# Performance work log

Hardware: AMD Instinct MI355X
Metric: run time of the kernel (lower is better)

Reference implementation:

```python
import jax, jax.numpy as jnp
import numpy as np

B, N, C, H = 16, 576, 768, 12
HD = C // H
SCALE = HD ** -0.5


def setup_inputs() -> dict:
    key = jax.random.key(0)
    ks = jax.random.split(key, 8)
    s = lambda fan: 1.0 / np.sqrt(fan)
    return {
        "x": jax.random.normal(ks[0], (B, N, C), jnp.float32),
        "Wqkv": jax.random.normal(ks[1], (3 * C, C), jnp.float32) * s(C),
        "Wl": jax.random.normal(ks[2], (H, H), jnp.float32) * s(H),
        "bl": jax.random.normal(ks[3], (H,), jnp.float32) * 0.02,
        "Ww": jax.random.normal(ks[4], (H, H), jnp.float32) * s(H),
        "bw": jax.random.normal(ks[5], (H,), jnp.float32) * 0.02,
        "Wproj": jax.random.normal(ks[6], (C, C), jnp.float32) * s(C),
        "bproj": jax.random.normal(ks[7], (C,), jnp.float32) * 0.02,
    }


def reference(x, Wqkv, Wl, bl, Ww, bw, Wproj, bproj):
    b, n, c = x.shape
    # qkv projection: (B,N,3C) -> (3,B,H,N,HD)
    qkv = (x @ Wqkv.T).reshape(b, n, 3, H, HD)
    qkv = jnp.transpose(qkv, (2, 0, 3, 1, 4))
    q, k, v = qkv[0] * SCALE, qkv[1], qkv[2]
    # raw scores (B,H,N,N)
    attn = jnp.einsum("bhmd,bhnd->bhmn", q, k)
    # talking-heads pre-softmax mix over head axis (nn.Linear: y = x @ W.T + b)
    attn = jnp.einsum("bhmn,gh->bgmn", attn, Wl) + bl[None, :, None, None]
    attn = jax.nn.softmax(attn, axis=-1)
    # talking-heads post-softmax mix
    attn = jnp.einsum("bhmn,gh->bgmn", attn, Ww) + bw[None, :, None, None]
    # attn @ V -> (B,N,C)
    out = jnp.einsum("bhmn,bhnd->bhmd", attn, v)
    out = jnp.transpose(out, (0, 2, 1, 3)).reshape(b, n, c)
    return out @ Wproj.T + bproj
```

## Files before the change

kernel.cpp:

```cpp
#include <hip/hip_runtime.h>

#define B_ 16
#define N_ 576
#define C_ 768
#define H_ 12
#define HD_ 64
#define M_ (B_*N_)
#define C3_ (3*C_)
#define KC_ 3
#define NT_ 18

typedef _Float16 f16;
typedef _Float16 f16x8 __attribute__((ext_vector_type(8)));
typedef _Float16 f16x4 __attribute__((ext_vector_type(4)));
typedef float f32x4 __attribute__((ext_vector_type(4)));
typedef float f32x2 __attribute__((ext_vector_type(2)));

__global__ void cvt_f32_f16(const float* __restrict__ in, f16* __restrict__ out, int n4) {
    int i = blockIdx.x * blockDim.x + threadIdx.x;
    int stride = gridDim.x * blockDim.x;
    for (; i < n4; i += stride) {
        float4 v = ((const float4*)in)[i];
        f16x4 o = { (f16)v.x, (f16)v.y, (f16)v.z, (f16)v.w };
        ((f16x4*)out)[i] = o;
    }
}

__device__ __forceinline__ int swz(int row, int slot) {
    return row * 32 + ((slot ^ ((row >> 1) & 3)) * 8);
}

__device__ __forceinline__ void gload16(const void* g, void* l) {
    __builtin_amdgcn_global_load_lds((const __attribute__((address_space(1))) void*)g,
                                     (__attribute__((address_space(3))) void*)l, 16, 0, 0);
}

__device__ __forceinline__ size_t qk_frag_off(int bh12, int t16, int half, int l) {
    return (((size_t)bh12 * 36 + t16) * 2 + half) * 512 + (size_t)l * 8;
}

__global__ __launch_bounds__(256) void gemm_qkv(const f16* __restrict__ A, const f16* __restrict__ Bw,
                                                f16* __restrict__ Qf, f16* __restrict__ Kf, f16* __restrict__ Vo) {
    __shared__ __align__(16) f16 lA[128 * 32];
    __shared__ __align__(16) f16 lB[128 * 32];
    __shared__ __align__(16) f16 eT[4][16][72];
    const int K = C_;
    int m0 = blockIdx.x * 128, n0 = blockIdx.y * 128;
    int t = threadIdx.x, lane = t & 63, wave = t >> 6;
    int wm = (wave >> 1) * 64, wn = (wave & 1) * 64;
    int srow0 = wave * 16 + (lane >> 2);
    int scol0 = ((lane & 3) ^ ((srow0 >> 1) & 3)) * 8;
    int srow1 = srow0 + 64;
    int scol1 = ((lane & 3) ^ ((srow1 >> 1) & 3)) * 8;
    f16* dA0 = lA + wave * 512 + lane * 8;
    f16* dA1 = lA + 2048 + wave * 512 + lane * 8;
    f16* dB0 = lB + wave * 512 + lane * 8;
    f16* dB1 = lB + 2048 + wave * 512 + lane * 8;
    const f16* A0 = A + (size_t)(m0 + srow0) * K + scol0;
    const f16* A1 = A + (size_t)(m0 + srow1) * K + scol1;
    const f16* B0 = Bw + (size_t)(n0 + srow0) * K + scol0;
    const f16* B1 = Bw + (size_t)(n0 + srow1) * K + scol1;
    f32x4 acc[4][4] = {};
    for (int k0 = 0; k0 < K; k0 += 32) {
        gload16(A0 + k0, dA0);
        gload16(A1 + k0, dA1);
        gload16(B0 + k0, dB0);
        gload16(B1 + k0, dB1);
        __syncthreads();
        f16x8 af[4], bf[4];
#pragma unroll
        for (int i = 0; i < 4; ++i) {
            af[i] = *(const f16x8*)(lA + swz(wm + i * 16 + (lane & 15), lane >> 4));
            bf[i] = *(const f16x8*)(lB + swz(wn + i * 16 + (lane & 15), lane >> 4));
        }
#pragma unroll
        for (int i = 0; i < 4; ++i)
#pragma unroll
            for (int j = 0; j < 4; ++j)
                acc[i][j] = __builtin_amdgcn_mfma_f32_16x16x32_f16(af[i], bf[j], acc[i][j], 0, 0, 0);
        __syncthreads();
    }
    int colw = n0 + wn;
    int tsel = colw / C_;
    int rem = colw - tsel * C_;
    int h = rem >> 6;
    float qs = (tsel == 0) ? 0.125f : 1.0f;
#pragma unroll
    for (int i = 0; i < 4; ++i) {
        int rowg = m0 + wm + i * 16;
        int bb = rowg / N_;
        int nnb = rowg - bb * N_;
        int bh = bb * H_ + h;
#pragma unroll
        for (int j = 0; j < 4; ++j)
#pragma unroll
            for (int r = 0; r < 4; ++r)
                eT[wave][(lane >> 4) * 4 + r][j * 16 + (lane & 15)] = (f16)(acc[i][j][r] * qs);
        if (tsel < 2) {
            f16* dst = (tsel == 0) ? Qf : Kf;
#pragma unroll
            for (int half = 0; half < 2; ++half) {
                f16x8 v = *(const f16x8*)&eT[wave][lane & 15][half * 32 + (lane >> 4) * 8];
                *(f16x8*)(dst + qk_frag_off(bh, nnb >> 4, half, lane)) = v;
            }
        } else {
#pragma unroll
            for (int hh = 0; hh < 2; ++hh) {
                int nl = hh * 8 + (lane >> 3);
                f16x8 v = *(const f16x8*)&eT[wave][nl][(lane & 7) * 8];
                *(f16x8*)(Vo + ((size_t)bh * N_ + nnb + nl) * HD_ + (lane & 7) * 8) = v;
            }
        }
    }
}

__global__ __launch_bounds__(256) void gemm_proj(const f16* __restrict__ A, const f16* __restrict__ Bw,
                                                 const float* __restrict__ bias, float* __restrict__ out) {
    __shared__ __align__(16) f16 lA[128 * 32];
    __shared__ __align__(16) f16 lB[128 * 32];
    const int K = C_;
    const size_t PSZ = (size_t)M_ * C_;
    int m0 = blockIdx.x * 128, n0 = blockIdx.y * 128;
    int t = threadIdx.x, lane = t & 63, wave = t >> 6;
    int wm = (wave >> 1) * 64, wn = (wave & 1) * 64;
    int srow = t >> 2, sslot = t & 3, scol = sslot * 8;
    f32x4 acc[4][4] = {};
    for (int k0 = 0; k0 < K; k0 += 32) {
        {
            size_t i0 = (size_t)(m0 + srow) * K + k0 + scol;
            size_t i1 = (size_t)(m0 + srow + 64) * K + k0 + scol;
            f16x8 a0 = *(const f16x8*)(A + i0), a1 = *(const f16x8*)(A + PSZ + i0), a2 = *(const f16x8*)(A + 2 * PSZ + i0);
            *(f16x8*)(lA + swz(srow, sslot)) = a0 + a1 + a2;
            f16x8 b0 = *(const f16x8*)(A + i1), b1 = *(const f16x8*)(A + PSZ + i1), b2 = *(const f16x8*)(A + 2 * PSZ + i1);
            *(f16x8*)(lA + swz(srow + 64, sslot)) = b0 + b1 + b2;
        }
        *(f16x8*)(lB + swz(srow,      sslot)) = *(const f16x8*)(Bw + (size_t)(n0 + srow)      * K + k0 + scol);
        *(f16x8*)(lB + swz(srow + 64, sslot)) = *(const f16x8*)(Bw + (size_t)(n0 + srow + 64) * K + k0 + scol);
        __syncthreads();
        f16x8 af[4], bf[4];
#pragma unroll
        for (int i = 0; i < 4; ++i) {
            af[i] = *(const f16x8*)(lA + swz(wm + i * 16 + (lane & 15), lane >> 4));
            bf[i] = *(const f16x8*)(lB + swz(wn + i * 16 + (lane & 15), lane >> 4));
        }
#pragma unroll
        for (int i = 0; i < 4; ++i)
#pragma unroll
            for (int j = 0; j < 4; ++j)
                acc[i][j] = __builtin_amdgcn_mfma_f32_16x16x32_f16(af[i], bf[j], acc[i][j], 0, 0, 0);
        __syncthreads();
    }
#pragma unroll
    for (int i = 0; i < 4; ++i) {
        int row0 = m0 + wm + i * 16 + ((lane >> 4) * 4);
#pragma unroll
        for (int j = 0; j < 4; ++j) {
            int col = n0 + wn + j * 16 + (lane & 15);
            float bv = bias[col];
#pragma unroll
            for (int r = 0; r < 4; ++r)
                out[(size_t)(row0 + r) * C_ + col] = acc[i][j][r] + bv;
        }
    }
}

__global__ void transpose_v(const f16* __restrict__ V, f16* __restrict__ Vf) {
    __shared__ f16 tile[64][68];
    int bh = blockIdx.y, n0 = blockIdx.x * 64;
    const f16* src = V + (size_t)bh * N_ * HD_;
    int t = threadIdx.x;
#pragma unroll
    for (int i = 0; i < 16; ++i) {
        int e = i * 256 + t;
        int r = e >> 6, c = e & 63;
        tile[r][c] = src[(size_t)(n0 + r) * HD_ + c];
    }
    __syncthreads();
#pragma unroll
    for (int i = 0; i < 2; ++i) {
        int u = i * 256 + t;
        int nt2 = u >> 8, dt = (u >> 6) & 3, l = u & 63;
        int nl = nt2 * 32 + ((l >> 4) << 3);
        int d = dt * 16 + (l & 15);
        f16x8 v;
#pragma unroll
        for (int j = 0; j < 8; ++j) v[j] = tile[nl + j][d];
        size_t off = (((size_t)bh * 18 + (n0 >> 5) + nt2) * 4 + dt) * 512 + (size_t)l * 8;
        *(f16x8*)(Vf + off) = v;
    }
}

__global__ __launch_bounds__(256) void scores_exp(const f16* __restrict__ Qf, const f16* __restrict__ Kf,
                                                  const float* __restrict__ Wl, const float* __restrict__ bl,
                                                  unsigned char* __restrict__ Sp, float* __restrict__ rps) {
    __shared__ float sWl[144];
    __shared__ float sbl[12];
    __shared__ float red[12][32][2];
    int fl = blockIdx.x;
    int xcd = fl & 7;
    int j = fl >> 3;
    int hi = (j >= 324) ? 1 : 0;
    int b = xcd * 2 + hi;
    int j2 = j - hi * 324;
    int p = j2 / 54;
    int rr2 = j2 - p * 54;
    int xt = p * 3 + (rr2 % 3);
    int yt = rr2 / 3;
    int t = threadIdx.x, lane = t & 63, wave = t >> 6;
    int mh = wave >> 1, nh = wave & 1;
    if (t < 144) sWl[t] = Wl[t];
    if (t >= 192 && t < 204) sbl[t - 192] = bl[t - 192];
    __syncthreads();
    int m16 = lane & 15, q = lane >> 4;
    int mt16 = xt * 2 + mh;
    int nt16 = yt * 2 + nh;
    f32x4 S[12];
#pragma unroll
    for (int h = 0; h < 12; ++h) {
        int bh = b * H_ + h;
        f16x8 k0 = *(const f16x8*)(Kf + qk_frag_off(bh, nt16, 0, lane));
        f16x8 k1 = *(const f16x8*)(Kf + qk_frag_off(bh, nt16, 1, lane));
        f16x8 q0 = *(const f16x8*)(Qf + qk_frag_off(bh, mt16, 0, lane));
        f16x8 q1 = *(const f16x8*)(Qf + qk_frag_off(bh, mt16, 1, lane));
        f32x4 a = {0.f, 0.f, 0.f, 0.f};
        a = __builtin_amdgcn_mfma_f32_16x16x32_f16(k0, q0, a, 0, 0, 0);
        a = __builtin_amdgcn_mfma_f32_16x16x32_f16(k1, q1, a, 0, 0, 0);
        S[h] = a;
    }
    int oct = nh * 2 + (q >> 1);
    int lp = m16 | (oct << 4);
    int jo = (q & 1) * 4;
    unsigned char* spb = Sp + ((((size_t)b * 36 + mt16) * 18 + yt) * 12) * 512 + lp * 8 + jo;
    float sg[12];
#pragma unroll
    for (int g = 0; g < 12; ++g) {
        float bg = sbl[g];
        f32x4 w = {bg, bg, bg, bg};
#pragma unroll
        for (int h = 0; h < 12; ++h) w += sWl[g * 12 + h] * S[h];
        float e0 = __expf(w[0]), e1 = __expf(w[1]), e2 = __expf(w[2]), e3 = __expf(w[3]);
        sg[g] = e0 + e1 + e2 + e3;
        unsigned int pk = 0;
        pk = __builtin_amdgcn_cvt_pk_fp8_f32(e0 * 0.25f, e1 * 0.25f, pk, false);
        pk = __builtin_amdgcn_cvt_pk_fp8_f32(e2 * 0.25f, e3 * 0.25f, pk, true);
        *(unsigned int*)(spb + g * 512) = pk;
    }
#pragma unroll
    for (int g = 0; g < 12; ++g) {
        float v = sg[g];
        v += __shfl_xor(v, 16, 64);
        v += __shfl_xor(v, 32, 64);
        if (lane < 16) red[g][mh * 16 + lane][nh] = v;
    }
    __syncthreads();
    for (int tt = t; tt < 384; tt += 256) {
        int g = tt >> 5, mr = tt & 31;
        float tot = red[g][mr][0] + red[g][mr][1];
        rps[(((size_t)b * H_ + g) * N_ + xt * 32 + mr) * NT_ + yt] = tot;
    }
}

__global__ __launch_bounds__(256) void sum_rinv(const float* __restrict__ rps, float* __restrict__ rinv) {
    int row = blockIdx.x * 256 + threadIdx.x;
    const float* p = rps + (size_t)row * NT_;
    float s = 0.f;
#pragma unroll
    for (int i = 0; i < NT_; ++i) s += p[i];
    rinv[row] = 1.0f / s;
}

__global__ __launch_bounds__(256) void pv_mix(const unsigned char* __restrict__ Sp, const f16* __restrict__ Vf,
                                              const float* __restrict__ Ww, const float* __restrict__ bw,
                                              const float* __restrict__ rinv, f16* __restrict__ Opart) {
    __shared__ float ils[12][16];
    int fl = blockIdx.x;
    int sw = (fl & 7) * 216 + (fl >> 3);
    int mt = sw % 36, rem = sw / 36;
    int b = rem & 15, kc = rem >> 4;
    int m0 = mt * 16;
    int t = threadIdx.x, lane = t & 63;
    int wv = __builtin_amdgcn_readfirstlane(t >> 6);
    if (t < 192) ils[t / 16][t % 16] = rinv[((size_t)b * H_ + t / 16) * N_ + m0 + (t % 16)];
    __syncthreads();
    int mrow = lane & 15, n8 = lane >> 4;
    float il_[12];
#pragma unroll
    for (int h = 0; h < 12; ++h) il_[h] = 4.0f * ils[h][mrow];
    float ww0[12], ww1[12], ww2[12];
#pragma unroll
    for (int h = 0; h < 12; ++h) {
        ww0[h] = Ww[(wv * 3 + 0) * H_ + h];
        ww1[h] = Ww[(wv * 3 + 1) * H_ + h];
        ww2[h] = Ww[(wv * 3 + 2) * H_ + h];
    }
    float bw0 = bw[wv * 3], bw1 = bw[wv * 3 + 1], bw2 = bw[wv * 3 + 2];
    const unsigned char* spf = Sp + (((size_t)b * 36 + mt) * 18 + kc * 6) * 6144;
    const f16* vfb = Vf + ((((size_t)b * 12 + wv * 3) * 18 + kc * 6) * 4) * 512;
    f32x4 O[3][4] = {};
    for (int it = 0; it < 6; ++it) {
        uint2 ck8[12];
#pragma unroll
        for (int c = 0; c < 12; ++c)
            ck8[c] = *(const uint2*)(spf + (size_t)(it * 12 + c) * 512 + lane * 8);
        float w0[8], w1[8], w2[8];
#pragma unroll
        for (int jj = 0; jj < 8; ++jj) { w0[jj] = bw0; w1[jj] = bw1; w2[jj] = bw2; }
#pragma unroll
        for (int h = 0; h < 12; ++h) {
            float il = il_[h];
            float c0 = ww0[h], c1 = ww1[h], c2 = ww2[h];
            f32x2 eA = __builtin_amdgcn_cvt_pk_f32_fp8(ck8[h].x, false);
            f32x2 eB = __builtin_amdgcn_cvt_pk_f32_fp8(ck8[h].x, true);
            f32x2 eC = __builtin_amdgcn_cvt_pk_f32_fp8(ck8[h].y, false);
            f32x2 eD = __builtin_amdgcn_cvt_pk_f32_fp8(ck8[h].y, true);
            float p0 = eA.x * il, p1 = eA.y * il, p2 = eB.x * il, p3 = eB.y * il;
            float p4 = eC.x * il, p5 = eC.y * il, p6 = eD.x * il, p7 = eD.y * il;
            w0[0] += c0 * p0; w0[1] += c0 * p1; w0[2] += c0 * p2; w0[3] += c0 * p3;
            w0[4] += c0 * p4; w0[5] += c0 * p5; w0[6] += c0 * p6; w0[7] += c0 * p7;
            w1[0] += c1 * p0; w1[1] += c1 * p1; w1[2] += c1 * p2; w1[3] += c1 * p3;
            w1[4] += c1 * p4; w1[5] += c1 * p5; w1[6] += c1 * p6; w1[7] += c1 * p7;
            w2[0] += c2 * p0; w2[1] += c2 * p1; w2[2] += c2 * p2; w2[3] += c2 * p3;
            w2[4] += c2 * p4; w2[5] += c2 * p5; w2[6] += c2 * p6; w2[7] += c2 * p7;
        }
        f16x8 af0, af1, af2;
#pragma unroll
        for (int jj = 0; jj < 8; ++jj) {
            af0[jj] = (f16)w0[jj]; af1[jj] = (f16)w1[jj]; af2[jj] = (f16)w2[jj];
        }
#pragma unroll
        for (int dt = 0; dt < 4; ++dt) {
            f16x8 bf0 = *(const f16x8*)(vfb + (size_t)0 * 36864 + it * 2048 + dt * 512 + lane * 8);
            O[0][dt] = __builtin_amdgcn_mfma_f32_16x16x32_f16(af0, bf0, O[0][dt], 0, 0, 0);
            f16x8 bf1 = *(const f16x8*)(vfb + (size_t)1 * 36864 + it * 2048 + dt * 512 + lane * 8);
            O[1][dt] = __builtin_amdgcn_mfma_f32_16x16x32_f16(af1, bf1, O[1][dt], 0, 0, 0);
            f16x8 bf2 = *(const f16x8*)(vfb + (size_t)2 * 36864 + it * 2048 + dt * 512 + lane * 8);
            O[2][dt] = __builtin_amdgcn_mfma_f32_16x16x32_f16(af2, bf2, O[2][dt], 0, 0, 0);
        }
    }
    f16* Ob = Opart + (size_t)kc * M_ * C_;
#pragma unroll
    for (int gi = 0; gi < 3; ++gi) {
        int g = wv * 3 + gi;
#pragma unroll
        for (int dt = 0; dt < 4; ++dt)
#pragma unroll
            for (int r = 0; r < 4; ++r)
                Ob[((size_t)b * N_ + m0 + n8 * 4 + r) * C_ + g * HD_ + dt * 16 + mrow] = (f16)O[gi][dt][r];
    }
}

extern "C" void kernel_launch(void* const* d_in, const int* in_sizes, int n_in,
                              void* d_out, int out_size, void* d_ws, size_t ws_size,
                              hipStream_t stream) {
    const float* x     = (const float*)d_in[0];
    const float* Wqkv  = (const float*)d_in[1];
    const float* Wl    = (const float*)d_in[2];
    const float* bl    = (const float*)d_in[3];
    const float* Ww    = (const float*)d_in[4];
    const float* bw    = (const float*)d_in[5];
    const float* Wproj = (const float*)d_in[6];
    const float* bproj = (const float*)d_in[7];
    float* out = (float*)d_out;

    char* ws = (char*)d_ws;
    size_t off = 0;
    auto alloc = [&](size_t bytes) -> void* {
        void* p = ws + off;
        off += (bytes + 255) & ~(size_t)255;
        return p;
    };
    f16* x_h  = (f16*)alloc((size_t)M_ * C_ * 2);
    f16* wq_h = (f16*)alloc((size_t)C3_ * C_ * 2);
    f16* wp_h = (f16*)alloc((size_t)C_ * C_ * 2);
    f16* qf_h = (f16*)alloc((size_t)B_ * H_ * N_ * HD_ * 2);
    f16* kf_h = (f16*)alloc((size_t)B_ * H_ * N_ * HD_ * 2);
    f16* v_h  = (f16*)alloc((size_t)B_ * H_ * N_ * HD_ * 2);
    f16* vf_h = (f16*)alloc((size_t)B_ * H_ * N_ * HD_ * 2);
    unsigned char* sp = (unsigned char*)alloc((size_t)B_ * N_ * N_ * 12);
    float* rps  = (float*)alloc((size_t)B_ * H_ * N_ * NT_ * 4);
    float* rinv = (float*)alloc((size_t)B_ * H_ * N_ * 4);
    f16* opart = (f16*)alloc((size_t)KC_ * M_ * C_ * 2);

    cvt_f32_f16<<<1024, 256, 0, stream>>>(x,     x_h,  M_ * C_ / 4);
    cvt_f32_f16<<<1024, 256, 0, stream>>>(Wqkv,  wq_h, C3_ * C_ / 4);
    cvt_f32_f16<<<512,  256, 0, stream>>>(Wproj, wp_h, C_ * C_ / 4);

    gemm_qkv<<<dim3(M_ / 128, C3_ / 128), 256, 0, stream>>>(x_h, wq_h, qf_h, kf_h, v_h);
    transpose_v<<<dim3(N_ / 64, B_ * H_), 256, 0, stream>>>(v_h, vf_h);
    scores_exp<<<5184, 256, 0, stream>>>(qf_h, kf_h, Wl, bl, sp, rps);
    sum_rinv<<<(B_ * H_ * N_) / 256, 256, 0, stream>>>(rps, rinv);
    pv_mix<<<36 * 16 * KC_, 256, 0, stream>>>(sp, vf_h, Ww, bw, rinv, opart);
    gemm_proj<<<dim3(M_ / 128, C_ / 128), 256, 0, stream>>>(opart, wp_h, bproj, out);
}
```

Baseline: 211.5 us.

## Stage K fragments in LDS for larger score tiles; async-load proj weights

The scores kernel moves to 512-thread blocks covering 64 query rows. Each block stages its 12 heads of K fragments in shared memory once and reuses them across four query tiles, instead of every wave reading K from global memory. The row-sum reduction buffer is switched to half precision to save shared memory, which may lose some accuracy in the softmax denominators. Separately, gemm_proj now loads its weight tiles with direct global-to-LDS loads rather than through registers, so those loads are issued earlier and no register staging is needed.

```diff
diff --git a/kernel.cpp b/kernel.cpp
--- a/kernel.cpp
+++ b/kernel.cpp
@@ -124,8 +124,18 @@
     int t = threadIdx.x, lane = t & 63, wave = t >> 6;
     int wm = (wave >> 1) * 64, wn = (wave & 1) * 64;
     int srow = t >> 2, sslot = t & 3, scol = sslot * 8;
+    int brow0 = wave * 16 + (lane >> 2);
+    int bcol0 = ((lane & 3) ^ ((brow0 >> 1) & 3)) * 8;
+    int brow1 = brow0 + 64;
+    int bcol1 = ((lane & 3) ^ ((brow1 >> 1) & 3)) * 8;
+    f16* dB0 = lB + wave * 512 + lane * 8;
+    f16* dB1 = lB + 2048 + wave * 512 + lane * 8;
+    const f16* B0 = Bw + (size_t)(n0 + brow0) * K + bcol0;
+    const f16* B1 = Bw + (size_t)(n0 + brow1) * K + bcol1;
     f32x4 acc[4][4] = {};
     for (int k0 = 0; k0 < K; k0 += 32) {
+        gload16(B0 + k0, dB0);
+        gload16(B1 + k0, dB1);
         {
             size_t i0 = (size_t)(m0 + srow) * K + k0 + scol;
             size_t i1 = (size_t)(m0 + srow + 64) * K + k0 + scol;
@@ -134,8 +144,6 @@
             f16x8 b0 = *(const f16x8*)(A + i1), b1 = *(const f16x8*)(A + PSZ + i1), b2 = *(const f16x8*)(A + 2 * PSZ + i1);
             *(f16x8*)(lA + swz(srow + 64, sslot)) = b0 + b1 + b2;
         }
-        *(f16x8*)(lB + swz(srow,      sslot)) = *(const f16x8*)(Bw + (size_t)(n0 + srow)      * K + k0 + scol);
-        *(f16x8*)(lB + swz(srow + 64, sslot)) = *(const f16x8*)(Bw + (size_t)(n0 + srow + 64) * K + k0 + scol);
         __syncthreads();
         f16x8 af[4], bf[4];
 #pragma unroll
@@ -190,36 +198,44 @@
     }
 }
 
-__global__ __launch_bounds__(256) void scores_exp(const f16* __restrict__ Qf, const f16* __restrict__ Kf,
+__global__ __launch_bounds__(512) void scores_exp(const f16* __restrict__ Qf, const f16* __restrict__ Kf,
                                                   const float* __restrict__ Wl, const float* __restrict__ bl,
                                                   unsigned char* __restrict__ Sp, float* __restrict__ rps) {
     __shared__ float sWl[144];
     __shared__ float sbl[12];
-    __shared__ float red[12][32][2];
+    __shared__ f16 red[12][64][2];
+    __shared__ __align__(16) f16 lK[2 * 12 * 2 * 512];
     int fl = blockIdx.x;
     int xcd = fl & 7;
     int j = fl >> 3;
-    int hi = (j >= 324) ? 1 : 0;
+    int hi = (j >= 162) ? 1 : 0;
     int b = xcd * 2 + hi;
-    int j2 = j - hi * 324;
-    int p = j2 / 54;
-    int rr2 = j2 - p * 54;
-    int xt = p * 3 + (rr2 % 3);
-    int yt = rr2 / 3;
+    int j2 = j - hi * 162;
+    int yt = j2 / 9;
+    int mb = j2 - yt * 9;
     int t = threadIdx.x, lane = t & 63, wave = t >> 6;
-    int mh = wave >> 1, nh = wave & 1;
+    int mh = wave >> 2 ? 0 : 0;
+    mh = wave >> 1;
+    int nh = wave & 1;
     if (t < 144) sWl[t] = Wl[t];
     if (t >= 192 && t < 204) sbl[t - 192] = bl[t - 192];
+#pragma unroll
+    for (int i = 0; i < 6; ++i) {
+        int c = wave * 6 + i;
+        int nh2 = c / 24, rest = c - nh2 * 24;
+        int h = rest >> 1, half = rest & 1;
+        gload16(Kf + qk_frag_off(b * H_ + h, yt * 2 + nh2, half, 0) + (size_t)lane * 8,
+                lK + c * 512 + lane * 8);
+    }
     __syncthreads();
     int m16 = lane & 15, q = lane >> 4;
-    int mt16 = xt * 2 + mh;
-    int nt16 = yt * 2 + nh;
+    int mt16 = mb * 4 + mh;
     f32x4 S[12];
 #pragma unroll
     for (int h = 0; h < 12; ++h) {
         int bh = b * H_ + h;
-        f16x8 k0 = *(const f16x8*)(Kf + qk_frag_off(bh, nt16, 0, lane));
-        f16x8 k1 = *(const f16x8*)(Kf + qk_frag_off(bh, nt16, 1, lane));
+        f16x8 k0 = *(const f16x8*)(lK + ((nh * 12 + h) * 2 + 0) * 512 + lane * 8);
+        f16x8 k1 = *(const f16x8*)(lK + ((nh * 12 + h) * 2 + 1) * 512 + lane * 8);
         f16x8 q0 = *(const f16x8*)(Qf + qk_frag_off(bh, mt16, 0, lane));
         f16x8 q1 = *(const f16x8*)(Qf + qk_frag_off(bh, mt16, 1, lane));
         f32x4 a = {0.f, 0.f, 0.f, 0.f};
@@ -250,13 +266,13 @@
         float v = sg[g];
         v += __shfl_xor(v, 16, 64);
         v += __shfl_xor(v, 32, 64);
-        if (lane < 16) red[g][mh * 16 + lane][nh] = v;
+        if (lane < 16) red[g][mh * 16 + lane][nh] = (f16)v;
     }
     __syncthreads();
-    for (int tt = t; tt < 384; tt += 256) {
-        int g = tt >> 5, mr = tt & 31;
-        float tot = red[g][mr][0] + red[g][mr][1];
-        rps[(((size_t)b * H_ + g) * N_ + xt * 32 + mr) * NT_ + yt] = tot;
+    for (int tt = t; tt < 768; tt += 512) {
+        int g = tt >> 6, mr = tt & 63;
+        float tot = (float)red[g][mr][0] + (float)red[g][mr][1];
+        rps[(((size_t)b * H_ + g) * N_ + mb * 64 + mr) * NT_ + yt] = tot;
     }
 }
 
@@ -387,7 +403,7 @@
 
     gemm_qkv<<<dim3(M_ / 128, C3_ / 128), 256, 0, stream>>>(x_h, wq_h, qf_h, kf_h, v_h);
     transpose_v<<<dim3(N_ / 64, B_ * H_), 256, 0, stream>>>(v_h, vf_h);
-    scores_exp<<<5184, 256, 0, stream>>>(qf_h, kf_h, Wl, bl, sp, rps);
+    scores_exp<<<2592, 512, 0, stream>>>(qf_h, kf_h, Wl, bl, sp, rps);
     sum_rinv<<<(B_ * H_ * N_) / 256, 256, 0, stream>>>(rps, rinv);
     pv_mix<<<36 * 16 * KC_, 256, 0, stream>>>(sp, vf_h, Ww, bw, rinv, opart);
     gemm_proj<<<dim3(M_ / 128, C_ / 128), 256, 0, stream>>>(opart, wp_h, bproj, out);
```

New measurement: 202.6 us. -4.2%, faster.
